# Performance work log

Hardware: AMD Instinct MI355X
Metric: run time of the kernel (lower is better)

The kernel has to match this reference:

```python
import jax, jax.numpy as jnp
import numpy as np

B, T, C, H = 2, 2048, 1024, 16
D = C // H  # head_dim = 64

def setup_inputs() -> dict:
    key = jax.random.key(0)
    k1, k2, k3, k4, k5 = jax.random.split(key, 5)
    x = jax.random.normal(k1, (B, T, C), dtype=jnp.float32)
    # RoPE tables (realistic frequencies)
    inv_freq = 1.0 / (10000.0 ** (jnp.arange(0, D // 2, dtype=jnp.float32) / (D // 2)))
    pos = jnp.arange(T, dtype=jnp.float32)
    ang = pos[:, None] * inv_freq[None, :]          # (T, D/2)
    cos, sin = jnp.cos(ang), jnp.sin(ang)
    # causal mask (True = keep)
    mask = jnp.tril(jnp.ones((T, T), dtype=bool))
    W_qkv = jax.random.normal(k2, (3 * C, C), dtype=jnp.float32) * (1.0 / np.sqrt(C))
    W_out = jax.random.normal(k3, (C, C), dtype=jnp.float32) * (1.0 / np.sqrt(C))
    return {"x": x, "cos": cos, "sin": sin, "mask": mask, "W_qkv": W_qkv, "W_out": W_out}

def apply_rope(x, cos, sin):
    # x: (B, H, T, D); cos/sin: (T, D/2)
    d = x.shape[-1] // 2
    x1, x2 = x[..., :d], x[..., d:]
    c = cos[None, None, :x.shape[2], :]
    s = sin[None, None, :x.shape[2], :]
    return jnp.concatenate([x1 * c - x2 * s, x2 * c + x1 * s], axis=-1)

def reference(x, cos, sin, mask, W_qkv, W_out):
    b, t, c = x.shape
    qkv = (x @ W_qkv.T).reshape(b, t, 3, H, D)
    q, k, v = qkv[:, :, 0], qkv[:, :, 1], qkv[:, :, 2]   # (b, t, H, D)
    q = q.transpose(0, 2, 1, 3)
    k = k.transpose(0, 2, 1, 3)
    v = v.transpose(0, 2, 1, 3)                           # (b, H, t, D)
    q = apply_rope(q, cos, sin)
    k = apply_rope(k, cos, sin)
    attn = jnp.einsum('bhqd,bhkd->bhqk', q, k) / jnp.sqrt(jnp.asarray(D, x.dtype))
    attn = jnp.where(mask[None, None, :, :], attn, -jnp.inf)
    attn = jax.nn.softmax(attn, axis=-1)
    out = jnp.einsum('bhqk,bhkd->bhqd', attn, v)          # (b, H, t, D)
    out = out.transpose(0, 2, 1, 3).reshape(b, t, c)
    return out @ W_out.T
```

## Files before the change

kernel.cpp:

```cpp
#include <hip/hip_runtime.h>
#include <stdint.h>

typedef __bf16 bf16;
typedef __bf16 bf16x4 __attribute__((ext_vector_type(4)));
typedef __bf16 bf16x8 __attribute__((ext_vector_type(8)));
typedef float f32x4 __attribute__((ext_vector_type(4)));

#define TSEQ 2048
#define NHEAD 16
#define HDIM 64
#define CDIM 1024

#define AS1(p) ((const __attribute__((address_space(1))) void*)(p))
#define AS3(p) ((__attribute__((address_space(3))) void*)(p))

#if __has_builtin(__builtin_amdgcn_exp2f)
#define EXP2(x) __builtin_amdgcn_exp2f(x)
#else
#define EXP2(x) exp2f(x)
#endif

__global__ __launch_bounds__(256) void cast3_bf16(const float* __restrict__ in1, int n1,
                                                  const float* __restrict__ in2, int n2,
                                                  const float* __restrict__ in3, int n3,
                                                  bf16* __restrict__ out1,
                                                  bf16* __restrict__ out2,
                                                  bf16* __restrict__ out3) {
  int i = (blockIdx.x * 256 + threadIdx.x) * 8;
  const float* src;
  bf16* dst;
  if (i < n1) {
    src = in1 + i; dst = out1 + i;
  } else if (i < n1 + n2) {
    src = in2 + (i - n1); dst = out2 + (i - n1);
  } else if (i < n1 + n2 + n3) {
    src = in3 + (i - n1 - n2); dst = out3 + (i - n1 - n2);
  } else {
    return;
  }
  float4 a = *(const float4*)src;
  float4 b = *(const float4*)(src + 4);
  bf16x8 r;
  r[0] = (bf16)a.x; r[1] = (bf16)a.y; r[2] = (bf16)a.z; r[3] = (bf16)a.w;
  r[4] = (bf16)b.x; r[5] = (bf16)b.y; r[6] = (bf16)b.z; r[7] = (bf16)b.w;
  *(bf16x8*)dst = r;
}

__global__ __launch_bounds__(256) void gemm_qkv_rope(const bf16* __restrict__ A,
                                                     const bf16* __restrict__ B,
                                                     const float* __restrict__ cosb,
                                                     const float* __restrict__ sinb,
                                                     bf16* __restrict__ Qb,
                                                     bf16* __restrict__ Kb,
                                                     bf16* __restrict__ Vt) {
  constexpr int K = 1024;
  __shared__ bf16 smem[24576];
  const int t = threadIdx.x;
  const int w = t >> 6, l = t & 63, g = l >> 4, ln = l & 15;
  const int wm = (w >> 1) * 64, wn = (w & 1) * 64;
  const int m0 = blockIdx.x * 128, n0 = blockIdx.y * 128;
  const int r0 = t >> 2, kc0 = (t & 3) * 8;

  f32x4 acc[4][4] = {};

#define STAGE_G1(buf, k0)                                                             \
  do {                                                                                \
    __builtin_amdgcn_global_load_lds(AS1(A + (size_t)(m0 + r0) * K + (k0) + kc0),     \
                                     AS3(&smem[(buf) * 8192 + t * 8]), 16, 0, 0);     \
    __builtin_amdgcn_global_load_lds(AS1(A + (size_t)(m0 + r0 + 64) * K + (k0) + kc0),\
                                     AS3(&smem[(buf) * 8192 + (t + 256) * 8]), 16, 0, 0); \
    __builtin_amdgcn_global_load_lds(AS1(B + (size_t)(n0 + r0) * K + (k0) + kc0),     \
                                     AS3(&smem[(buf) * 8192 + 4096 + t * 8]), 16, 0, 0);  \
    __builtin_amdgcn_global_load_lds(AS1(B + (size_t)(n0 + r0 + 64) * K + (k0) + kc0),\
                                     AS3(&smem[(buf) * 8192 + 4096 + (t + 256) * 8]), 16, 0, 0); \
  } while (0)

  STAGE_G1(0, 0);
  STAGE_G1(1, 32);
  asm volatile("s_waitcnt vmcnt(4) lgkmcnt(0)" ::: "memory");
  __builtin_amdgcn_s_barrier();
  asm volatile("" ::: "memory");

  for (int it = 0; it < 32; ++it) {
    const int cur = it % 3;
    if (it < 30) STAGE_G1((it + 2) % 3, (it + 2) * 32);
    const bf16* sa = &smem[cur * 8192];
    const bf16* sb = &smem[cur * 8192 + 4096];
    bf16x8 af[4], bfr[4];
#pragma unroll
    for (int i = 0; i < 4; i++) {
      af[i] = *(const bf16x8*)&sa[(wm + i * 16 + ln) * 32 + g * 8];
      bfr[i] = *(const bf16x8*)&sb[(wn + i * 16 + ln) * 32 + g * 8];
    }
#pragma unroll
    for (int i = 0; i < 4; i++)
#pragma unroll
      for (int j = 0; j < 4; j++)
        acc[i][j] = __builtin_amdgcn_mfma_f32_16x16x32_bf16(af[i], bfr[j], acc[i][j], 0, 0, 0);
    if (it < 30) {
      asm volatile("s_waitcnt vmcnt(4) lgkmcnt(0)" ::: "memory");
      __builtin_amdgcn_s_barrier();
      asm volatile("" ::: "memory");
    } else if (it == 30) {
      asm volatile("s_waitcnt vmcnt(0) lgkmcnt(0)" ::: "memory");
      __builtin_amdgcn_s_barrier();
      asm volatile("" ::: "memory");
    }
  }
#undef STAGE_G1

  const int part = n0 >> 10;
  if (part < 2) {
    bf16* dst = part ? Kb : Qb;
    const float qs = part ? 1.0f : 0.18033688011112042f;
#pragma unroll
    for (int i = 0; i < 4; i++)
#pragma unroll
      for (int j = 0; j < 2; j++) {
        int nl = (n0 & 1023) + wn + j * 16 + ln;
        int h = nl >> 6, d = nl & 31;
#pragma unroll
        for (int r = 0; r < 4; r++) {
          int row = m0 + wm + i * 16 + g * 4 + r;
          int tok = row & (TSEQ - 1), bb = row >> 11;
          float c = cosb[tok * 32 + d], s = sinb[tok * 32 + d];
          float a1 = acc[i][j][r], a2 = acc[i][j + 2][r];
          size_t ob = ((size_t)(bb * NHEAD + h) * TSEQ + tok) * HDIM + d;
          dst[ob] = (bf16)((a1 * c - a2 * s) * qs);
          dst[ob + 32] = (bf16)((a2 * c + a1 * s) * qs);
        }
      }
  } else {
    const int bb = m0 >> 11;
    const int tbase = m0 & (TSEQ - 1);
    const int nbase = n0 - 2048;
#pragma unroll
    for (int pass = 0; pass < 2; pass++) {
      __syncthreads();
      if ((w >> 1) == pass) {
#pragma unroll
        for (int i = 0; i < 4; i++)
#pragma unroll
          for (int j = 0; j < 4; j++) {
            int lr = i * 16 + g * 4;
            int lc = wn + j * 16 + ln;
#pragma unroll
            for (int r = 0; r < 4; r++)
              smem[(lr + r) * 132 + lc] = (bf16)acc[i][j][r];
          }
      }
      __syncthreads();
      for (int c = t; c < 1024; c += 256) {
        int ch = c >> 3, tc = c & 7;
        bf16x8 o;
#pragma unroll
        for (int j2 = 0; j2 < 8; j2++) o[j2] = smem[(tc * 8 + j2) * 132 + ch];
        int n = nbase + ch;
        int h = n >> 6, d = n & 63;
        *(bf16x8*)(Vt + ((size_t)((bb * NHEAD + h) * HDIM + d)) * TSEQ +
                   tbase + pass * 64 + tc * 8) = o;
      }
    }
  }
}

__global__ __launch_bounds__(256) void gemm_out(const bf16* __restrict__ A,
                                                const bf16* __restrict__ B,
                                                float* __restrict__ C,
                                                int M, int N, int K) {
  __shared__ bf16 smem[8192];
  const int t = threadIdx.x;
  const int w = t >> 6, l = t & 63, g = l >> 4, ln = l & 15;
  const int wm = (w >> 1) * 64, wn = (w & 1) * 64;
  const int m0 = blockIdx.x * 128, n0 = blockIdx.y * 128;
  const int r0 = t >> 2, kc0 = (t & 3) * 8;

  f32x4 acc[4][4] = {};

  for (int k0 = 0; k0 < K; k0 += 32) {
    __syncthreads();
    __builtin_amdgcn_global_load_lds(AS1(A + (size_t)(m0 + r0) * K + k0 + kc0),
                                     AS3(&smem[t * 8]), 16, 0, 0);
    __builtin_amdgcn_global_load_lds(AS1(A + (size_t)(m0 + r0 + 64) * K + k0 + kc0),
                                     AS3(&smem[(t + 256) * 8]), 16, 0, 0);
    __builtin_amdgcn_global_load_lds(AS1(B + (size_t)(n0 + r0) * K + k0 + kc0),
                                     AS3(&smem[4096 + t * 8]), 16, 0, 0);
    __builtin_amdgcn_global_load_lds(AS1(B + (size_t)(n0 + r0 + 64) * K + k0 + kc0),
                                     AS3(&smem[4096 + (t + 256) * 8]), 16, 0, 0);
    __syncthreads();
    bf16x8 af[4], bfr[4];
#pragma unroll
    for (int i = 0; i < 4; i++) {
      af[i] = *(const bf16x8*)&smem[(wm + i * 16 + ln) * 32 + g * 8];
      bfr[i] = *(const bf16x8*)&smem[4096 + (wn + i * 16 + ln) * 32 + g * 8];
    }
#pragma unroll
    for (int i = 0; i < 4; i++)
#pragma unroll
      for (int j = 0; j < 4; j++)
        acc[i][j] = __builtin_amdgcn_mfma_f32_16x16x32_bf16(af[i], bfr[j], acc[i][j], 0, 0, 0);
  }
#pragma unroll
  for (int i = 0; i < 4; i++)
#pragma unroll
    for (int j = 0; j < 4; j++) {
      int row = m0 + wm + i * 16 + g * 4;
      int col = n0 + wn + j * 16 + ln;
#pragma unroll
      for (int r = 0; r < 4; r++)
        C[(size_t)(row + r) * N + col] = acc[i][j][r];
    }
}

__global__ __launch_bounds__(1024, 4) void attn_fwd(const bf16* __restrict__ Q,
                                                    const bf16* __restrict__ K,
                                                    const bf16* __restrict__ Vt,
                                                    bf16* __restrict__ ctx) {
  __shared__ __align__(16) char smem_raw[65536];
  bf16* Ks = (bf16*)smem_raw;
  bf16* VTs = (bf16*)(smem_raw + 16384);
  bf16* Ps = (bf16*)(smem_raw + 32768);
  float* Mbuf = (float*)smem_raw;
  float* Lbuf = (float*)(smem_raw + 32768);

  const int t = threadIdx.x;
  const int w = t >> 6;
  const int p = w >> 3;
  const int wq = w & 7;
  const int l = t & 63, g = l >> 4, ln = l & 15;
  const int bid = blockIdx.x;
  const int bh = bid & 31;
  const int qb0 = 15 - (bid >> 5);
  const size_t base = (size_t)bh * TSEQ * HDIM;

  const int q0 = qb0 * 128;
  const int qwb = q0 + wq * 16;
  const int dtile = qwb >> 6;
  const int q_g = qwb + ln;
  const int lswz = (ln & 7) * 8;

  const int ts = t >> 9;
  const int tt = t & 511;
  const int r0 = tt >> 3, ch0 = (tt & 7) * 8;
  const int sidx = r0 * 64 + (((tt & 7) ^ (r0 & 7)) * 8);

  bf16x8 bq[2];
  bq[0] = *(const bf16x8*)(Q + base + (size_t)q_g * HDIM + g * 8);
  bq[1] = *(const bf16x8*)(Q + base + (size_t)q_g * HDIM + 32 + g * 8);

  const bf16* kp = K + base + (size_t)(ts * 64 + r0) * HDIM + ch0;
  const bf16* vp = Vt + base + (size_t)r0 * TSEQ + ts * 64 + ch0;
  bf16x8 kr = *(const bf16x8*)kp;
  bf16x8 vr = *(const bf16x8*)vp;

  f32x4 acc[4] = {};
  float l_run = 0.f;

  for (int i = 0; i <= qb0; i++) {
    __syncthreads();
    *(bf16x8*)&Ks[ts * 4096 + sidx] = kr;
    *(bf16x8*)&VTs[ts * 4096 + sidx] = vr;
    __syncthreads();
    if (i < qb0) {
      kr = *(const bf16x8*)(kp + (size_t)(i + 1) * 128 * HDIM);
      vr = *(const bf16x8*)(vp + (i + 1) * 128);
    }
    const int kt = 2 * i + p;
    if (kt <= dtile) {
      f32x4 st[4] = {};
      __builtin_amdgcn_s_setprio(1);
#pragma unroll
      for (int step = 0; step < 2; step++)
#pragma unroll
        for (int mt = 0; mt < 4; mt++) {
          bf16x8 ak = *(const bf16x8*)&Ks[p * 4096 + (mt * 16 + ln) * 64 +
                                          ((step * 32 + g * 8) ^ lswz)];
          st[mt] = __builtin_amdgcn_mfma_f32_16x16x32_bf16(ak, bq[step], st[mt], 0, 0, 0);
        }
      __builtin_amdgcn_s_setprio(0);
      float vals[16];
      if (kt == dtile) {
#pragma unroll
        for (int mt = 0; mt < 4; mt++)
#pragma unroll
          for (int r = 0; r < 4; r++) {
            int kg = kt * 64 + mt * 16 + g * 4 + r;
            vals[mt * 4 + r] = (kg <= q_g) ? st[mt][r] : -INFINITY;
          }
      } else {
#pragma unroll
        for (int mt = 0; mt < 4; mt++)
#pragma unroll
          for (int r = 0; r < 4; r++) vals[mt * 4 + r] = st[mt][r];
      }
      float psum = 0.f;
#pragma unroll
      for (int i2 = 0; i2 < 16; i2++) {
        float pv = EXP2(vals[i2]);
        vals[i2] = pv;
        psum += pv;
      }
      psum += __shfl_xor(psum, 16);
      psum += __shfl_xor(psum, 32);
      l_run += psum;
#pragma unroll
      for (int mt = 0; mt < 4; mt++) {
        bf16x4 pk;
#pragma unroll
        for (int r = 0; r < 4; r++) pk[r] = (bf16)vals[mt * 4 + r];
        *(bf16x4*)&Ps[w * 1024 + ln * 64 +
                      (((mt * 16 + (g >> 1) * 8) ^ lswz) + (g & 1) * 4)] = pk;
      }
      __builtin_amdgcn_s_setprio(1);
#pragma unroll
      for (int step = 0; step < 2; step++) {
        bf16x8 ap = *(const bf16x8*)&Ps[w * 1024 + ln * 64 + ((step * 32 + g * 8) ^ lswz)];
#pragma unroll
        for (int nt = 0; nt < 4; nt++) {
          bf16x8 bv = *(const bf16x8*)&VTs[p * 4096 + (nt * 16 + ln) * 64 +
                                           ((step * 32 + g * 8) ^ lswz)];
          acc[nt] = __builtin_amdgcn_mfma_f32_16x16x32_bf16(ap, bv, acc[nt], 0, 0, 0);
        }
      }
      __builtin_amdgcn_s_setprio(0);
    }
  }

  __syncthreads();
  if (p == 1) {
#pragma unroll
    for (int nt = 0; nt < 4; nt++)
      *(f32x4*)&Mbuf[(wq * 64 + l) * 16 + nt * 4] = acc[nt];
    Lbuf[wq * 64 + l] = l_run;
  }
  __syncthreads();
  if (p == 0) {
#pragma unroll
    for (int nt = 0; nt < 4; nt++) acc[nt] += *(const f32x4*)&Mbuf[(wq * 64 + l) * 16 + nt * 4];
    l_run += Lbuf[wq * 64 + l];
    float inv = 1.0f / l_run;
    float lrow[4];
#pragma unroll
    for (int r = 0; r < 4; r++) lrow[r] = __shfl(inv, g * 4 + r, 64);
    const int b = bh >> 4, h = bh & (NHEAD - 1);
#pragma unroll
    for (int nt = 0; nt < 4; nt++)
#pragma unroll
      for (int r = 0; r < 4; r++) {
        int q = qwb + g * 4 + r;
        ctx[(size_t)(b * TSEQ + q) * CDIM + h * HDIM + nt * 16 + ln] =
            (bf16)(acc[nt][r] * lrow[r]);
      }
  }
}

extern "C" void kernel_launch(void* const* d_in, const int* in_sizes, int n_in,
                              void* d_out, int out_size, void* d_ws, size_t ws_size,
                              hipStream_t stream) {
  const float* x = (const float*)d_in[0];
  const float* cosb = (const float*)d_in[1];
  const float* sinb = (const float*)d_in[2];
  const float* Wqkv = (const float*)d_in[4];
  const float* Wout = (const float*)d_in[5];
  float* out = (float*)d_out;

  char* ws = (char*)d_ws;
  bf16* x_bf = (bf16*)ws;
  bf16* ctx = (bf16*)ws;
  bf16* Wqkv_bf = (bf16*)(ws + 8388608);
  bf16* Wout_bf = (bf16*)(ws + 14680064);
  bf16* Qb = (bf16*)(ws + 16777216);
  bf16* Kb = (bf16*)(ws + 25165824);
  bf16* Vt = (bf16*)(ws + 33554432);

  cast3_bf16<<<(4194304 + 3145728 + 1048576) / 8 / 256, 256, 0, stream>>>(
      x, 4194304, Wqkv, 3145728, Wout, 1048576, x_bf, Wqkv_bf, Wout_bf);
  gemm_qkv_rope<<<dim3(32, 24), 256, 0, stream>>>(x_bf, Wqkv_bf, cosb, sinb, Qb, Kb, Vt);
  attn_fwd<<<512, 1024, 0, stream>>>(Qb, Kb, Vt, ctx);
  gemm_out<<<dim3(32, 8), 256, 0, stream>>>(ctx, Wout_bf, out, 4096, 1024, 1024);
}
```

Baseline: 185.3 us.

## Triple-buffer output projection GEMM with async LDS loads and vmcnt waits

Converts the output-projection GEMM's single-buffered LDS loop into a three-stage pipeline. The next two K-tiles are prefetched with global_load_lds while the current tile runs MFMAs, and explicit vmcnt waits with barriers replace the two syncthreads per iteration. The goal is to hide global-load latency behind compute. In exchange, LDS use triples to 48KB, the loop count is hardcoded to K=1024, and correctness relies on the manual waitcnt accounting.

After: 178.2 us. 1.04x faster.

```diff
diff --git a/kernel.cpp b/kernel.cpp
--- a/kernel.cpp
+++ b/kernel.cpp
@@ -168,7 +168,7 @@
                                                 const bf16* __restrict__ B,
                                                 float* __restrict__ C,
                                                 int M, int N, int K) {
-  __shared__ bf16 smem[8192];
+  __shared__ bf16 smem[24576];
   const int t = threadIdx.x;
   const int w = t >> 6, l = t & 63, g = l >> 4, ln = l & 15;
   const int wm = (w >> 1) * 64, wn = (w & 1) * 64;
@@ -177,29 +177,52 @@
 
   f32x4 acc[4][4] = {};
 
-  for (int k0 = 0; k0 < K; k0 += 32) {
-    __syncthreads();
-    __builtin_amdgcn_global_load_lds(AS1(A + (size_t)(m0 + r0) * K + k0 + kc0),
-                                     AS3(&smem[t * 8]), 16, 0, 0);
-    __builtin_amdgcn_global_load_lds(AS1(A + (size_t)(m0 + r0 + 64) * K + k0 + kc0),
-                                     AS3(&smem[(t + 256) * 8]), 16, 0, 0);
-    __builtin_amdgcn_global_load_lds(AS1(B + (size_t)(n0 + r0) * K + k0 + kc0),
-                                     AS3(&smem[4096 + t * 8]), 16, 0, 0);
-    __builtin_amdgcn_global_load_lds(AS1(B + (size_t)(n0 + r0 + 64) * K + k0 + kc0),
-                                     AS3(&smem[4096 + (t + 256) * 8]), 16, 0, 0);
-    __syncthreads();
+#define STAGE_GO(buf, k0)                                                             \
+  do {                                                                                \
+    __builtin_amdgcn_global_load_lds(AS1(A + (size_t)(m0 + r0) * K + (k0) + kc0),     \
+                                     AS3(&smem[(buf) * 8192 + t * 8]), 16, 0, 0);     \
+    __builtin_amdgcn_global_load_lds(AS1(A + (size_t)(m0 + r0 + 64) * K + (k0) + kc0),\
+                                     AS3(&smem[(buf) * 8192 + (t + 256) * 8]), 16, 0, 0); \
+    __builtin_amdgcn_global_load_lds(AS1(B + (size_t)(n0 + r0) * K + (k0) + kc0),     \
+                                     AS3(&smem[(buf) * 8192 + 4096 + t * 8]), 16, 0, 0);  \
+    __builtin_amdgcn_global_load_lds(AS1(B + (size_t)(n0 + r0 + 64) * K + (k0) + kc0),\
+                                     AS3(&smem[(buf) * 8192 + 4096 + (t + 256) * 8]), 16, 0, 0); \
+  } while (0)
+
+  STAGE_GO(0, 0);
+  STAGE_GO(1, 32);
+  asm volatile("s_waitcnt vmcnt(4) lgkmcnt(0)" ::: "memory");
+  __builtin_amdgcn_s_barrier();
+  asm volatile("" ::: "memory");
+
+  for (int it = 0; it < 32; ++it) {
+    const int cur = it % 3;
+    if (it < 30) STAGE_GO((it + 2) % 3, (it + 2) * 32);
+    const bf16* sa = &smem[cur * 8192];
+    const bf16* sb = &smem[cur * 8192 + 4096];
     bf16x8 af[4], bfr[4];
 #pragma unroll
     for (int i = 0; i < 4; i++) {
-      af[i] = *(const bf16x8*)&smem[(wm + i * 16 + ln) * 32 + g * 8];
-      bfr[i] = *(const bf16x8*)&smem[4096 + (wn + i * 16 + ln) * 32 + g * 8];
+      af[i] = *(const bf16x8*)&sa[(wm + i * 16 + ln) * 32 + g * 8];
+      bfr[i] = *(const bf16x8*)&sb[(wn + i * 16 + ln) * 32 + g * 8];
     }
 #pragma unroll
     for (int i = 0; i < 4; i++)
 #pragma unroll
       for (int j = 0; j < 4; j++)
         acc[i][j] = __builtin_amdgcn_mfma_f32_16x16x32_bf16(af[i], bfr[j], acc[i][j], 0, 0, 0);
-  }
+    if (it < 30) {
+      asm volatile("s_waitcnt vmcnt(4) lgkmcnt(0)" ::: "memory");
+      __builtin_amdgcn_s_barrier();
+      asm volatile("" ::: "memory");
+    } else if (it == 30) {
+      asm volatile("s_waitcnt vmcnt(0) lgkmcnt(0)" ::: "memory");
+      __builtin_amdgcn_s_barrier();
+      asm volatile("" ::: "memory");
+    }
+  }
+#undef STAGE_GO
+
 #pragma unroll
   for (int i = 0; i < 4; i++)
 #pragma unroll
```
